# Optimization experiments

Hardware: AMD Instinct MI355X
Metric: run time of the kernel (lower is better)

Reference implementation:

```python
import jax, jax.numpy as jnp
import numpy as np
from jax.ops import segment_sum, segment_max

H, D, HID, L, B = 4, 32, 128, 2, 64  # heads, head_dim, hidden, layers, graphs
NB, NS, NC, NF = 100000, 20000, 10000, 2000


def setup_inputs() -> dict:
    key = jax.random.key(0)
    ks = iter(jax.random.split(key, 64))
    nrm = lambda shape, s=1.0: jax.random.normal(next(ks), shape, jnp.float32) * s
    ridx = lambda n, hi: jax.random.randint(next(ks), (n,), 0, hi, jnp.int32)
    srt = lambda n, hi: jnp.sort(jax.random.randint(next(ks), (n,), 0, hi, jnp.int32))
    return {
        'x_block': nrm((NB, 8)), 'x_spmt': nrm((NS, 10)),
        'x_crane': nrm((NC, 7)), 'x_facility': nrm((NF, 3)),
        'Wp_b': nrm((8, HID), 0.2), 'bp_b': jnp.zeros((HID,), jnp.float32),
        'Wp_s': nrm((10, HID), 0.2), 'bp_s': jnp.zeros((HID,), jnp.float32),
        'Wp_c': nrm((7, HID), 0.2), 'bp_c': jnp.zeros((HID,), jnp.float32),
        'Wp_f': nrm((3, HID), 0.2), 'bp_f': jnp.zeros((HID,), jnp.float32),
        'gat_W': nrm((L, 8, HID, HID), 0.05),
        'gat_as': nrm((L, 8, H, D), 0.1), 'gat_ad': nrm((L, 8, H, D), 0.1),
        'gat_b': jnp.zeros((L, 8, HID), jnp.float32),
        'ln_s': jnp.ones((L, HID), jnp.float32), 'ln_b': jnp.zeros((L, HID), jnp.float32),
        'e_nt_s': ridx(800000, NB), 'e_nt_d': ridx(800000, NS),
        'e_ct_s': ridx(800000, NS), 'e_ct_d': ridx(800000, NB),
        'e_nl_s': ridx(400000, NB), 'e_nl_d': ridx(400000, NC),
        'e_cl_s': ridx(400000, NC), 'e_cl_d': ridx(400000, NB),
        'e_ba_s': ridx(100000, NB), 'e_ba_d': ridx(100000, NF),
        'e_pr_s': ridx(800000, NB), 'e_pr_d': ridx(800000, NB),
        'e_sa_s': ridx(20000, NS), 'e_sa_d': ridx(20000, NF),
        'e_ca_s': ridx(10000, NC), 'e_ca_d': ridx(10000, NF),
        'b_block': srt(NB, B), 'b_spmt': srt(NS, B),
        'b_crane': srt(NC, B), 'b_facility': srt(NF, B),
    }


def layer_norm(x, s, b):
    mu = x.mean(-1, keepdims=True)
    v = ((x - mu) ** 2).mean(-1, keepdims=True)
    return (x - mu) / jnp.sqrt(v + 1e-5) * s + b


def gat(h_src, h_dst, src, dst, W, a_s, a_d, bias):
    # PyG GATConv (shared lin for src/dst, add_self_loops=False, eval mode)
    n_dst = h_dst.shape[0]
    hs = (h_src @ W).reshape(-1, H, D)                 # [Ns,H,D]
    hd = (h_dst @ W).reshape(-1, H, D)                 # [Nd,H,D]
    al_s = (hs * a_s).sum(-1)                          # [Ns,H]
    al_d = (hd * a_d).sum(-1)                          # [Nd,H]
    e = jax.nn.leaky_relu(al_s[src] + al_d[dst], 0.2)  # [E,H]
    m = segment_max(e, dst, num_segments=n_dst)
    m = jnp.where(jnp.isfinite(m), m, 0.0)             # empty segments
    ex = jnp.exp(e - m[dst])
    den = segment_sum(ex, dst, num_segments=n_dst)
    coef = ex / (den[dst] + 1e-16)                     # scatter-softmax
    msg = hs[src] * coef[..., None]                    # [E,H,D]
    out = segment_sum(msg, dst, num_segments=n_dst)
    return out.reshape(n_dst, H * D) + bias


def pool(x, b):
    s = segment_sum(x, b, num_segments=B)
    c = segment_sum(jnp.ones((x.shape[0],), x.dtype), b, num_segments=B)
    return s / jnp.clip(c, 1.0)[:, None]


def reference(x_block, x_spmt, x_crane, x_facility,
              Wp_b, bp_b, Wp_s, bp_s, Wp_c, bp_c, Wp_f, bp_f,
              gat_W, gat_as, gat_ad, gat_b, ln_s, ln_b,
              e_nt_s, e_nt_d, e_ct_s, e_ct_d, e_nl_s, e_nl_d, e_cl_s, e_cl_d,
              e_ba_s, e_ba_d, e_pr_s, e_pr_d, e_sa_s, e_sa_d, e_ca_s, e_ca_d,
              b_block, b_spmt, b_crane, b_facility):
    xb = x_block @ Wp_b + bp_b
    xs = x_spmt @ Wp_s + bp_s
    xc = x_crane @ Wp_c + bp_c
    xf = x_facility @ Wp_f + bp_f
    rels = [(0, 'b', 's', e_nt_s, e_nt_d), (1, 's', 'b', e_ct_s, e_ct_d),
            (2, 'b', 'c', e_nl_s, e_nl_d), (3, 'c', 'b', e_cl_s, e_cl_d),
            (4, 'b', 'f', e_ba_s, e_ba_d), (5, 'b', 'b', e_pr_s, e_pr_d),
            (6, 's', 'f', e_sa_s, e_sa_d), (7, 'c', 'f', e_ca_s, e_ca_d)]
    for l in range(L):
        x = {'b': xb, 's': xs, 'c': xc, 'f': xf}
        acc = {k: [] for k in x}
        for r, st, dt, src, dst in rels:
            acc[dt].append(gat(x[st], x[dt], src, dst,
                               gat_W[l, r], gat_as[l, r], gat_ad[l, r], gat_b[l, r]))
        new = {k: sum(v) / len(v) for k, v in acc.items()}  # HeteroConv mean
        xb = layer_norm(jax.nn.relu(new['b']) + xb, ln_s[l], ln_b[l])
        xs = layer_norm(jax.nn.relu(new['s']) + xs, ln_s[l], ln_b[l])
        xc = layer_norm(jax.nn.relu(new['c']) + xc, ln_s[l], ln_b[l])
        xf = layer_norm(jax.nn.relu(new['f']) + xf, ln_s[l], ln_b[l])
    return jnp.concatenate([pool(xb, b_block), pool(xs, b_spmt),
                            pool(xc, b_crane), pool(xf, b_facility)], axis=-1)
```

## Files before the change

### kernel.cpp

```cpp
#include <hip/hip_runtime.h>
#include <hip/hip_bf16.h>
#include <cstdint>

#define HID 128
#define NHEAD 4
#define NGRAPH 64
#define PCHUNK 32

typedef __attribute__((ext_vector_type(8))) short bf16x8;
typedef __attribute__((ext_vector_type(4))) short bf16x4s;
typedef __attribute__((ext_vector_type(4))) float f32x4;

__device__ __forceinline__ float bf2f(short u) {
    union { float f; unsigned int i; } c;
    c.i = ((unsigned int)(unsigned short)u) << 16;
    return c.f;
}
__device__ __forceinline__ float lrelu(float a) { return (a > 0.f) ? a : 0.2f * a; }

struct PrePack {
    const int* edst[8]; int* deg[8]; int E[8]; int h_off[9];
    const float* px[4]; const float* pW[4]; const float* pb[4]; float* po[4];
    int pN[4]; int pK[4]; int p_off[5];
    const float* gat_W; __hip_bfloat16* Wsw;
    const float* gat_as; const float* gat_ad; float* vecall;
};

__global__ __launch_bounds__(256) void k_pre(PrePack A) {
    int b = blockIdx.x;
    int tid = threadIdx.x;
    if (b < A.h_off[8]) {
#pragma unroll
        for (int r = 0; r < 8; ++r) {
            if (b >= A.h_off[r] && b < A.h_off[r + 1]) {
                int e = (b - A.h_off[r]) * 256 + tid;
                if (e < A.E[r]) atomicAdd(&A.deg[r][A.edst[r][e]], 1);
            }
        }
        return;
    }
    b -= A.h_off[8];
    if (b < A.p_off[4]) {
#pragma unroll
        for (int t = 0; t < 4; ++t) {
            if (b >= A.p_off[t] && b < A.p_off[t + 1]) {
                int idx = (b - A.p_off[t]) * 256 + tid;
                if (idx < A.pN[t] * HID) {
                    int row = idx >> 7, c = idx & 127;
                    int K = A.pK[t];
                    float acc = A.pb[t][c];
                    for (int k = 0; k < K; ++k) acc += A.px[t][row * K + k] * A.pW[t][k * HID + c];
                    A.po[t][idx] = acc;
                }
            }
        }
        return;
    }
    b -= A.p_off[4];
    if (b < 1024) {
        int idx = b * 256 + tid;
        int l = idx >> 17;
        int rem = idx & 131071;
        int k = rem >> 10;
        int gc = rem & 1023;
        int rel, n, gobase, Ncols;
        if (gc < 512) {
            int i = gc >> 7;
            rel = (i == 0) ? 0 : (i == 1) ? 2 : (i == 2) ? 4 : 5;
            n = gc; gobase = 0; Ncols = 512;
        } else if (gc < 768) {
            int c2 = gc - 512;
            rel = (c2 >> 7) ? 6 : 1;
            n = c2; gobase = 65536; Ncols = 256;
        } else {
            int c2 = gc - 768;
            rel = (c2 >> 7) ? 7 : 3;
            n = c2; gobase = 98304; Ncols = 256;
        }
        int nl = n & 127;
        float v = A.gat_W[(((size_t)l * 8 + rel) * 128 + k) * 128 + nl];
        size_t dst = (size_t)l * 131072 + gobase + ((size_t)(k >> 3) * Ncols + n) * 8 + (k & 7);
        A.Wsw[dst] = __float2bfloat16(v);
        return;
    }
    b -= 1024;
    {
        int idx = b * 256 + tid;
        if (idx < 16384) {
            int h = idx & 3, k = (idx >> 2) & 127, p = (idx >> 9) & 15, l = idx >> 13;
            int r = p >> 1, side = p & 1;
            const float* W = A.gat_W + (((size_t)l * 8 + r) * 128 + k) * 128;
            const float* a = (side ? A.gat_ad : A.gat_as) + ((size_t)l * 8 + r) * 128;
            float s = 0.f;
#pragma unroll
            for (int j = 0; j < 32; ++j) s += W[h * 32 + j] * a[h * 32 + j];
            A.vecall[((size_t)l * 16 + p) * 512 + k * 4 + h] = s;
        }
    }
}

struct CsrPack {
    const int* esrc[8];
    const int* edst[8];
    int* deg[8];
    int* offs[8];
    int* curs[8];
    int* adj[8];
    int E[8];
    int Nd[8];
};

__global__ void k_scan_part_all(CsrPack P, int* __restrict__ part_all) {
    int r = blockIdx.y;
    int N = P.Nd[r];
    if (blockIdx.x * 256 >= N) return;
    __shared__ int sh[256];
    int t = threadIdx.x, i = blockIdx.x * 256 + t;
    sh[t] = (i < N) ? P.deg[r][i] : 0;
    __syncthreads();
    for (int o = 128; o; o >>= 1) {
        if (t < o) sh[t] += sh[t + o];
        __syncthreads();
    }
    if (t == 0) part_all[r * 512 + blockIdx.x] = sh[0];
}
__global__ void k_scan_top_all(int* __restrict__ part_all, CsrPack P) {
    int r = blockIdx.x;
    int n = (P.Nd[r] + 255) / 256;
    __shared__ int sh[512];
    int t = threadIdx.x;
    int v = (t < n) ? part_all[r * 512 + t] : 0;
    sh[t] = v;
    __syncthreads();
    for (int o = 1; o < 512; o <<= 1) {
        int tmp = (t >= o) ? sh[t - o] : 0;
        __syncthreads();
        sh[t] += tmp;
        __syncthreads();
    }
    if (t < n) part_all[r * 512 + t] = sh[t] - v;
}
__global__ void k_scan_down_all(CsrPack P, const int* __restrict__ part_all) {
    int r = blockIdx.y;
    int N = P.Nd[r];
    if (blockIdx.x * 256 >= N) return;
    __shared__ int sh[256];
    int t = threadIdx.x, i = blockIdx.x * 256 + t;
    int v = (i < N) ? P.deg[r][i] : 0;
    sh[t] = v;
    __syncthreads();
    for (int o = 1; o < 256; o <<= 1) {
        int tmp = (t >= o) ? sh[t - o] : 0;
        __syncthreads();
        sh[t] += tmp;
        __syncthreads();
    }
    if (i < N) {
        int excl = sh[t] - v + part_all[r * 512 + blockIdx.x];
        P.offs[r][i] = excl;
        P.curs[r][i] = excl;
    }
}

struct BinPack {
    const int* esrc[8]; const int* edst[8];
    uint2* staging[8];
    int* curs[8]; int* adj[8];
    int* binCnt; int* binBase; int* binCur;
    int E[8]; int Nd[8]; int binshift[8];
};

__global__ void k_binscan(BinPack B, const int* __restrict__ part_all) {
    int r = threadIdx.x;
    if (r >= 8) return;
    int cnt[8];
#pragma unroll
    for (int b = 0; b < 8; ++b) cnt[b] = 0;
    int nparts = (B.Nd[r] + 255) >> 8;
    int cshift = B.binshift[r] - 8;
    for (int c = 0; c < nparts; ++c) cnt[c >> cshift] += part_all[r * 512 + c];
    int run = 0;
    for (int b = 0; b < 8; ++b) {
        B.binCnt[r * 8 + b] = cnt[b];
        B.binBase[r * 8 + b] = run;
        B.binCur[r * 8 + b] = run;
        run += cnt[b];
    }
}

__global__ __launch_bounds__(256) void k_binp1(BinPack B) {
    int r = blockIdx.y;
    int E = B.E[r];
    int sh = B.binshift[r];
    __shared__ int h[8], base[8], rk[8];
    int tid = threadIdx.x;
    for (int e0 = blockIdx.x * 256; e0 < E; e0 += gridDim.x * 256) {
        if (tid < 8) { h[tid] = 0; rk[tid] = 0; }
        __syncthreads();
        int e = e0 + tid;
        int valid = e < E;
        int src = 0, dst = 0, bin = 0;
        if (valid) {
            src = B.esrc[r][e];
            dst = B.edst[r][e];
            bin = dst >> sh;
            atomicAdd(&h[bin], 1);
        }
        __syncthreads();
        if (tid < 8 && h[tid] > 0) base[tid] = atomicAdd(&B.binCur[r * 8 + tid], h[tid]);
        __syncthreads();
        if (valid) {
            int pos = base[bin] + atomicAdd(&rk[bin], 1);
            B.staging[r][pos] = make_uint2((unsigned)src, (unsigned)dst);
        }
        __syncthreads();
    }
}

__global__ __launch_bounds__(256) void k_binp2(BinPack B) {
    int r = blockIdx.y;
    int bin = blockIdx.x & 7;
    int cstart = blockIdx.x >> 3;
    int nstride = gridDim.x >> 3;
    int cnt = B.binCnt[r * 8 + bin];
    const uint2* st = B.staging[r] + B.binBase[r * 8 + bin];
    int* curs = B.curs[r];
    int* adj = B.adj[r];
    for (int i0 = cstart * 256; i0 < cnt; i0 += nstride * 256) {
        int i = i0 + threadIdx.x;
        if (i < cnt) {
            uint2 ed = st[i];
            int slot = atomicAdd(&curs[ed.y], 1);
            adj[slot] = (int)ed.x;
        }
    }
}

__device__ __forceinline__ void gemm_body(char* smemraw, const float* __restrict__ A,
                                          const __hip_bfloat16* __restrict__ Bsw,
                                          __hip_bfloat16* __restrict__ out,
                                          int M, int Ncols, int bx, int by) {
    __hip_bfloat16 (*Alds)[136] = (__hip_bfloat16 (*)[136])smemraw;
    int m0 = bx * 64, n0 = by * 128;
    int t = threadIdx.x;
    for (int i = t; i < 2048; i += 256) {
        int row = i >> 5, ch = i & 31;
        float4 v = make_float4(0.f, 0.f, 0.f, 0.f);
        if (m0 + row < M) v = *(const float4*)(A + (size_t)(m0 + row) * 128 + ch * 4);
        __hip_bfloat16* dp = &Alds[row][ch * 4];
        dp[0] = __float2bfloat16(v.x);
        dp[1] = __float2bfloat16(v.y);
        dp[2] = __float2bfloat16(v.z);
        dp[3] = __float2bfloat16(v.w);
    }
    __syncthreads();
    int w = t >> 6, l = t & 63;
    int lane16 = l & 15, q = l >> 4;
    f32x4 acc[8];
#pragma unroll
    for (int nn = 0; nn < 8; ++nn) acc[nn] = (f32x4){0.f, 0.f, 0.f, 0.f};
    const __hip_bfloat16* arow = &Alds[w * 16 + lane16][q * 8];
#pragma unroll
    for (int kk = 0; kk < 4; ++kk) {
        bf16x8 a = *(const bf16x8*)(arow + kk * 32);
#pragma unroll
        for (int nn = 0; nn < 8; ++nn) {
            size_t boff = ((size_t)(kk * 4 + q) * Ncols + (n0 + nn * 16 + lane16)) * 8;
            bf16x8 b = *(const bf16x8*)(Bsw + boff);
            acc[nn] = __builtin_amdgcn_mfma_f32_16x16x32_bf16(a, b, acc[nn], 0, 0, 0);
        }
    }
    int orow = m0 + w * 16 + q * 4;
#pragma unroll
    for (int nn = 0; nn < 8; ++nn) {
        int col = n0 + nn * 16 + lane16;
#pragma unroll
        for (int r = 0; r < 4; ++r) {
            int row = orow + r;
            if (row < M) out[(size_t)row * Ncols + col] = __float2bfloat16(acc[nn][r]);
        }
    }
}

__device__ __forceinline__ void logits_body(char* smemraw,
                                            const float* const vec[7], float* const outp[7],
                                            const float* __restrict__ x, int N, int nv, int bloc) {
    float (*vs)[128][4] = (float (*)[128][4])smemraw;
    int t = threadIdx.x;
    for (int i = t; i < nv * 512; i += 256) {
        int v = i >> 9, j = i & 511;
        vs[v][j >> 2][j & 3] = vec[v][j];
    }
    __syncthreads();
    int nl = t >> 2, h = t & 3;
    int node = bloc * 64 + nl;
    if (node >= N) return;
    const float* xr = x + (size_t)node * 128;
    float acc[7];
#pragma unroll
    for (int v = 0; v < 7; ++v) acc[v] = 0.f;
#pragma unroll 4
    for (int k = 0; k < 128; ++k) {
        float xv = xr[k];
#pragma unroll
        for (int v = 0; v < 7; ++v)
            if (v < nv) acc[v] += xv * vs[v][k][h];
    }
#pragma unroll
    for (int v = 0; v < 7; ++v)
        if (v < nv) outp[v][node * 4 + h] = acc[v];
}

struct MidPack {
    const float* gA[3]; const __hip_bfloat16* gB[3]; __hip_bfloat16* gO[3];
    int gM[3]; int gNc[3]; int gMB[3]; int g_off[4];
    const float* lvec[4][7]; float* lout[4][7]; const float* lx[4];
    int lN[4]; int lnv[4]; int l_off[5];
};

__global__ __launch_bounds__(256) void k_mid(MidPack M) {
    __shared__ __align__(16) char smem[17408];
    int b = blockIdx.x;
    if (b < M.g_off[3]) {
#pragma unroll
        for (int g = 0; g < 3; ++g) {
            if (b >= M.g_off[g] && b < M.g_off[g + 1]) {
                int local = b - M.g_off[g];
                int bx = local % M.gMB[g];
                int by = local / M.gMB[g];
                gemm_body(smem, M.gA[g], M.gB[g], M.gO[g], M.gM[g], M.gNc[g], bx, by);
            }
        }
        return;
    }
    b -= M.g_off[3];
#pragma unroll
    for (int t = 0; t < 4; ++t) {
        if (b >= M.l_off[t] && b < M.l_off[t + 1]) {
            logits_body(smem, M.lvec[t], M.lout[t], M.lx[t], M.lN[t], M.lnv[t], b - M.l_off[t]);
        }
    }
}

struct RelArg {
    const __hip_bfloat16* hs;
    int hstride;
    int hoff;
    const float* als;
    const float* ald;
    const int* adj;
    const int* off;
    const int* deg;
    const float* bias;
};

__device__ __forceinline__ void dst_body(const RelArg& r0, const RelArg& r1, const RelArg& r2,
                                         int nrel, float inv_nrel, float* __restrict__ x,
                                         const float* __restrict__ ln_s,
                                         const float* __restrict__ ln_b, int N, int bloc) {
    int wv = threadIdx.x >> 6, lane = threadIdx.x & 63;
    int half = lane >> 5, sl = lane & 31;
    int d = bloc * 8 + wv * 2 + half;
    if (d >= N) return;
    int c0 = sl * 4;
    int h = sl >> 3;
    float4 xv = *(const float4*)&x[(size_t)d * HID + c0];
    float rel0 = 0.f, rel1 = 0.f, rel2 = 0.f, rel3 = 0.f;
    for (int rr = 0; rr < nrel; ++rr) {
        const RelArg& R = (rr == 0) ? r0 : (rr == 1) ? r1 : r2;
        int base = R.off[d];
        int dg = R.deg[d];
        float aldh = R.ald[d * NHEAD + h];
        const __hip_bfloat16* hp = R.hs + R.hoff + c0;
        const int hstr = R.hstride;
        const int* ap = R.adj + base;
        const float* als = R.als;
        float a0 = 0.f, a1 = 0.f, a2 = 0.f, a3 = 0.f, den = 0.f;
        int k = 0;
        for (; k + 4 <= dg; k += 4) {
            int s0 = ap[k], s1 = ap[k + 1], s2 = ap[k + 2], s3 = ap[k + 3];
            float w0 = __expf(lrelu(als[s0 * NHEAD + h] + aldh));
            float w1 = __expf(lrelu(als[s1 * NHEAD + h] + aldh));
            float w2 = __expf(lrelu(als[s2 * NHEAD + h] + aldh));
            float w3 = __expf(lrelu(als[s3 * NHEAD + h] + aldh));
            bf16x4s v0 = *(const bf16x4s*)(hp + (size_t)s0 * hstr);
            bf16x4s v1 = *(const bf16x4s*)(hp + (size_t)s1 * hstr);
            bf16x4s v2 = *(const bf16x4s*)(hp + (size_t)s2 * hstr);
            bf16x4s v3 = *(const bf16x4s*)(hp + (size_t)s3 * hstr);
            a0 += w0 * bf2f(v0[0]) + w1 * bf2f(v1[0]) + w2 * bf2f(v2[0]) + w3 * bf2f(v3[0]);
            a1 += w0 * bf2f(v0[1]) + w1 * bf2f(v1[1]) + w2 * bf2f(v2[1]) + w3 * bf2f(v3[1]);
            a2 += w0 * bf2f(v0[2]) + w1 * bf2f(v1[2]) + w2 * bf2f(v2[2]) + w3 * bf2f(v3[2]);
            a3 += w0 * bf2f(v0[3]) + w1 * bf2f(v1[3]) + w2 * bf2f(v2[3]) + w3 * bf2f(v3[3]);
            den += w0 + w1 + w2 + w3;
        }
        for (; k < dg; ++k) {
            int s = ap[k];
            float w = __expf(lrelu(als[s * NHEAD + h] + aldh));
            bf16x4s v = *(const bf16x4s*)(hp + (size_t)s * hstr);
            a0 += w * bf2f(v[0]);
            a1 += w * bf2f(v[1]);
            a2 += w * bf2f(v[2]);
            a3 += w * bf2f(v[3]);
            den += w;
        }
        float inv = 1.f / (den + 1e-16f);
        rel0 += a0 * inv + R.bias[c0];
        rel1 += a1 * inv + R.bias[c0 + 1];
        rel2 += a2 * inv + R.bias[c0 + 2];
        rel3 += a3 * inv + R.bias[c0 + 3];
    }
    float v0 = rel0 * inv_nrel, v1 = rel1 * inv_nrel;
    float v2 = rel2 * inv_nrel, v3 = rel3 * inv_nrel;
    v0 = (v0 > 0.f) ? v0 : 0.f;
    v1 = (v1 > 0.f) ? v1 : 0.f;
    v2 = (v2 > 0.f) ? v2 : 0.f;
    v3 = (v3 > 0.f) ? v3 : 0.f;
    v0 += xv.x; v1 += xv.y; v2 += xv.z; v3 += xv.w;
    float s = v0 + v1 + v2 + v3;
    float ss = v0 * v0 + v1 * v1 + v2 * v2 + v3 * v3;
#pragma unroll
    for (int o = 16; o; o >>= 1) {
        s += __shfl_xor(s, o);
        ss += __shfl_xor(ss, o);
    }
    float mu = s * (1.f / HID);
    float var = ss * (1.f / HID) - mu * mu;
    float rstd = rsqrtf(var + 1e-5f);
    float o0 = (v0 - mu) * rstd * ln_s[c0] + ln_b[c0];
    float o1 = (v1 - mu) * rstd * ln_s[c0 + 1] + ln_b[c0 + 1];
    float o2 = (v2 - mu) * rstd * ln_s[c0 + 2] + ln_b[c0 + 2];
    float o3 = (v3 - mu) * rstd * ln_s[c0 + 3] + ln_b[c0 + 3];
    *(float4*)&x[(size_t)d * HID + c0] = make_float4(o0, o1, o2, o3);
}

struct TypeArg {
    RelArg r0, r1, r2;
    float* x;
    int N;
    int nrel;
    float inv_nrel;
};

__global__ __launch_bounds__(256) void k_dst_all(TypeArg t0, TypeArg t1, TypeArg t2, TypeArg t3,
                                                 int off1, int off2, int off3,
                                                 const float* __restrict__ ln_s,
                                                 const float* __restrict__ ln_b) {
    int b = blockIdx.x;
    if (b < off1) {
        dst_body(t0.r0, t0.r1, t0.r2, t0.nrel, t0.inv_nrel, t0.x, ln_s, ln_b, t0.N, b);
    } else if (b < off2) {
        dst_body(t1.r0, t1.r1, t1.r2, t1.nrel, t1.inv_nrel, t1.x, ln_s, ln_b, t1.N, b - off1);
    } else if (b < off3) {
        dst_body(t2.r0, t2.r1, t2.r2, t2.nrel, t2.inv_nrel, t2.x, ln_s, ln_b, t2.N, b - off2);
    } else {
        dst_body(t3.r0, t3.r1, t3.r2, t3.nrel, t3.inv_nrel, t3.x, ln_s, ln_b, t3.N, b - off3);
    }
}

__global__ void k_pool_all(const float* __restrict__ x0, const float* __restrict__ x1,
                           const float* __restrict__ x2, const float* __restrict__ x3,
                           const int* __restrict__ b0, const int* __restrict__ b1,
                           const int* __restrict__ b2, const int* __restrict__ b3,
                           int N0, int N1, int N2, int N3, float* __restrict__ out) {
    int ty = blockIdx.y;
    const float* x;
    const int* b;
    int N, toff;
    if (ty == 0)      { x = x0; b = b0; N = N0; toff = 0; }
    else if (ty == 1) { x = x1; b = b1; N = N1; toff = 128; }
    else if (ty == 2) { x = x2; b = b2; N = N2; toff = 256; }
    else              { x = x3; b = b3; N = N3; toff = 384; }
    int r0 = blockIdx.x * PCHUNK;
    if (r0 >= N) return;
    int rend = min(r0 + PCHUNK, N);
    int c = threadIdx.x;
    int cur = b[r0];
    float acc = 0.f;
    for (int i = r0; i < rend; ++i) {
        int g = b[i];
        if (g != cur) {
            atomicAdd(&out[cur * 512 + toff + c], acc);
            acc = 0.f;
            cur = g;
        }
        acc += x[(size_t)i * HID + c];
    }
    atomicAdd(&out[cur * 512 + toff + c], acc);
}
__global__ void k_cnt(const int* __restrict__ b0, const int* __restrict__ b1,
                      const int* __restrict__ b2, const int* __restrict__ b3,
                      int N0, int N1, int N2, int N3, float* __restrict__ cnt) {
    int i = blockIdx.x * blockDim.x + threadIdx.x;
    if (i >= 256) return;
    int t = i >> 6, g = i & 63;
    const int* b = (t == 0) ? b0 : (t == 1) ? b1 : (t == 2) ? b2 : b3;
    int N = (t == 0) ? N0 : (t == 1) ? N1 : (t == 2) ? N2 : N3;
    int lo = 0, hi = N;
    while (lo < hi) { int m = (lo + hi) >> 1; if (b[m] < g) lo = m + 1; else hi = m; }
    int s = lo;
    hi = N;
    while (lo < hi) { int m = (lo + hi) >> 1; if (b[m] < g + 1) lo = m + 1; else hi = m; }
    cnt[i] = (float)(lo - s);
}
__global__ void k_div(float* __restrict__ out, const float* __restrict__ cnt) {
    int idx = blockIdx.x * blockDim.x + threadIdx.x;
    if (idx >= NGRAPH * 512) return;
    int g = idx >> 9, c = idx & 511, t = c >> 7;
    out[idx] = out[idx] / fmaxf(cnt[t * NGRAPH + g], 1.0f);
}

extern "C" void kernel_launch(void* const* d_in, const int* in_sizes, int n_in,
                              void* d_out, int out_size, void* d_ws, size_t ws_size,
                              hipStream_t stream) {
    const float* x_in[4] = {(const float*)d_in[0], (const float*)d_in[1],
                            (const float*)d_in[2], (const float*)d_in[3]};
    const float* Wp[4] = {(const float*)d_in[4], (const float*)d_in[6],
                          (const float*)d_in[8], (const float*)d_in[10]};
    const float* bp[4] = {(const float*)d_in[5], (const float*)d_in[7],
                          (const float*)d_in[9], (const float*)d_in[11]};
    const float* gat_W  = (const float*)d_in[12];
    const float* gat_as = (const float*)d_in[13];
    const float* gat_ad = (const float*)d_in[14];
    const float* gat_b  = (const float*)d_in[15];
    const float* ln_s   = (const float*)d_in[16];
    const float* ln_b   = (const float*)d_in[17];
    const int* esrc[8] = {(const int*)d_in[18], (const int*)d_in[20], (const int*)d_in[22],
                          (const int*)d_in[24], (const int*)d_in[26], (const int*)d_in[28],
                          (const int*)d_in[30], (const int*)d_in[32]};
    const int* edst[8] = {(const int*)d_in[19], (const int*)d_in[21], (const int*)d_in[23],
                          (const int*)d_in[25], (const int*)d_in[27], (const int*)d_in[29],
                          (const int*)d_in[31], (const int*)d_in[33]};
    const int* bidx[4] = {(const int*)d_in[34], (const int*)d_in[35],
                          (const int*)d_in[36], (const int*)d_in[37]};
    int E[8];
    {
        const int eidx[8] = {18, 20, 22, 24, 26, 28, 30, 32};
        for (int r = 0; r < 8; ++r) E[r] = in_sizes[eidx[r]];
    }
    const int Kin[4] = {8, 10, 7, 3};
    int N[4];
    for (int t = 0; t < 4; ++t) N[t] = in_sizes[t] / Kin[t];
    const int rel_st[8] = {0, 1, 0, 2, 0, 0, 1, 2};
    const int rel_dt[8] = {1, 0, 2, 0, 3, 0, 3, 3};
    const int rel_hoff[8] = {0, 0, 128, 0, 256, 384, 128, 128};
    const int grp_stride[4] = {512, 256, 256, 0};
    (void)ws_size; (void)n_in;

    char* wbase = (char*)d_ws;
    size_t cur = 0;
    auto alloc = [&](size_t bytes) -> void* {
        void* p = wbase + cur;
        cur += (bytes + 15) & ~(size_t)15;
        return p;
    };
    float* x[4];
    for (int t = 0; t < 4; ++t) x[t] = (float*)alloc((size_t)N[t] * HID * 4);
    __hip_bfloat16* hs_g[3];
    hs_g[0] = (__hip_bfloat16*)alloc((size_t)N[0] * 512 * 2);
    hs_g[1] = (__hip_bfloat16*)alloc((size_t)N[1] * 256 * 2);
    hs_g[2] = (__hip_bfloat16*)alloc((size_t)N[2] * 256 * 2);
    __hip_bfloat16* Wsw = (__hip_bfloat16*)alloc((size_t)2 * 131072 * 2);
    float* vecall = (float*)alloc((size_t)2 * 16 * 512 * 4);
    float *als_[8], *ald_[8];
    int *deg[8], *offs[8], *curs[8], *adj[8];
    uint2* staging[8];
    int NdTot = 0;
    for (int r = 0; r < 8; ++r) NdTot += N[rel_dt[r]] + 4;
    int* deg_all = (int*)alloc((size_t)NdTot * 4);
    {
        int off = 0;
        for (int r = 0; r < 8; ++r) { deg[r] = deg_all + off; off += N[rel_dt[r]] + 4; }
    }
    for (int r = 0; r < 8; ++r) {
        int Ns = N[rel_st[r]], Nd = N[rel_dt[r]];
        als_[r] = (float*)alloc((size_t)Ns * NHEAD * 4);
        ald_[r] = (float*)alloc((size_t)Nd * NHEAD * 4);
        offs[r] = (int*)alloc((size_t)Nd * 4);
        curs[r] = (int*)alloc((size_t)Nd * 4);
        adj[r]  = (int*)alloc((size_t)E[r] * 4);
        staging[r] = (uint2*)alloc((size_t)E[r] * 8);
    }
    int* part_all = (int*)alloc(8 * 512 * 4);
    int* binCnt   = (int*)alloc(64 * 4);
    int* binBase  = (int*)alloc(64 * 4);
    int* binCur   = (int*)alloc(64 * 4);
    float* cntf   = (float*)alloc(256 * 4);

    CsrPack CP;
    int NdMax = 0, Emax = 0;
    for (int r = 0; r < 8; ++r) {
        CP.esrc[r] = esrc[r]; CP.edst[r] = edst[r];
        CP.deg[r] = deg[r]; CP.offs[r] = offs[r]; CP.curs[r] = curs[r]; CP.adj[r] = adj[r];
        CP.E[r] = E[r]; CP.Nd[r] = N[rel_dt[r]];
        if (CP.Nd[r] > NdMax) NdMax = CP.Nd[r];
        if (E[r] > Emax) Emax = E[r];
    }
    BinPack BP;
    for (int r = 0; r < 8; ++r) {
        BP.esrc[r] = esrc[r]; BP.edst[r] = edst[r];
        BP.staging[r] = staging[r];
        BP.curs[r] = curs[r]; BP.adj[r] = adj[r];
        BP.E[r] = E[r]; BP.Nd[r] = N[rel_dt[r]];
        int sh = 8;
        while (((BP.Nd[r] - 1) >> sh) > 7) ++sh;
        BP.binshift[r] = sh;
    }
    BP.binCnt = binCnt; BP.binBase = binBase; BP.binCur = binCur;

    hipMemsetAsync(deg_all, 0, (size_t)NdTot * 4, stream);
    PrePack PA;
    {
        for (int r = 0; r < 8; ++r) { PA.edst[r] = edst[r]; PA.deg[r] = deg[r]; PA.E[r] = E[r]; }
        PA.h_off[0] = 0;
        for (int r = 0; r < 8; ++r) PA.h_off[r + 1] = PA.h_off[r] + (E[r] + 255) / 256;
        for (int t = 0; t < 4; ++t) {
            PA.px[t] = x_in[t]; PA.pW[t] = Wp[t]; PA.pb[t] = bp[t]; PA.po[t] = x[t];
            PA.pN[t] = N[t]; PA.pK[t] = Kin[t];
        }
        PA.p_off[0] = 0;
        for (int t = 0; t < 4; ++t) PA.p_off[t + 1] = PA.p_off[t] + (N[t] * HID + 255) / 256;
        PA.gat_W = gat_W; PA.Wsw = Wsw;
        PA.gat_as = gat_as; PA.gat_ad = gat_ad; PA.vecall = vecall;
        int total = PA.h_off[8] + PA.p_off[4] + 1024 + 64;
        k_pre<<<total, 256, 0, stream>>>(PA);
    }

    {
        dim3 gn((NdMax + 255) / 256, 8);
        k_scan_part_all<<<gn, 256, 0, stream>>>(CP, part_all);
        k_binscan<<<1, 64, 0, stream>>>(BP, part_all);
        k_scan_top_all<<<8, 512, 0, stream>>>(part_all, CP);
        k_scan_down_all<<<gn, 256, 0, stream>>>(CP, part_all);
        dim3 g1(512, 8);
        k_binp1<<<g1, 256, 0, stream>>>(BP);
        dim3 g2(512, 8);
        k_binp2<<<g2, 256, 0, stream>>>(BP);
    }

    hipMemsetAsync(d_out, 0, (size_t)out_size * 4, stream);
    k_cnt<<<1, 256, 0, stream>>>(bidx[0], bidx[1], bidx[2], bidx[3],
                                 N[0], N[1], N[2], N[3], cntf);

    const size_t g_woff[3] = {0, 65536, 98304};
    const int g_ncols[3] = {512, 256, 256};
    int nb[4];
    for (int t = 0; t < 4; ++t) nb[t] = (N[t] + 7) / 8;
    int doff1 = nb[0], doff2 = nb[0] + nb[1], doff3 = nb[0] + nb[1] + nb[2];
    int dtot = doff3 + nb[3];

    for (int l = 0; l < 2; ++l) {
        MidPack M;
        M.g_off[0] = 0;
        for (int g = 0; g < 3; ++g) {
            M.gA[g] = x[g];
            M.gB[g] = Wsw + (size_t)l * 131072 + g_woff[g];
            M.gO[g] = hs_g[g];
            M.gM[g] = N[g];
            M.gNc[g] = g_ncols[g];
            M.gMB[g] = (N[g] + 63) / 64;
            M.g_off[g + 1] = M.g_off[g] + M.gMB[g] * (g_ncols[g] / 128);
        }
        const float* vl = vecall + (size_t)l * 16 * 512;
        auto vvec = [&](int r, int side) { return vl + (size_t)(r * 2 + side) * 512; };
        for (int t = 0; t < 4; ++t)
            for (int v = 0; v < 7; ++v) { M.lvec[t][v] = vl; M.lout[t][v] = als_[0]; }
        M.lvec[0][0] = vvec(0, 0); M.lout[0][0] = als_[0];
        M.lvec[0][1] = vvec(2, 0); M.lout[0][1] = als_[2];
        M.lvec[0][2] = vvec(4, 0); M.lout[0][2] = als_[4];
        M.lvec[0][3] = vvec(5, 0); M.lout[0][3] = als_[5];
        M.lvec[0][4] = vvec(1, 1); M.lout[0][4] = ald_[1];
        M.lvec[0][5] = vvec(3, 1); M.lout[0][5] = ald_[3];
        M.lvec[0][6] = vvec(5, 1); M.lout[0][6] = ald_[5];
        M.lvec[1][0] = vvec(1, 0); M.lout[1][0] = als_[1];
        M.lvec[1][1] = vvec(6, 0); M.lout[1][1] = als_[6];
        M.lvec[1][2] = vvec(0, 1); M.lout[1][2] = ald_[0];
        M.lvec[2][0] = vvec(3, 0); M.lout[2][0] = als_[3];
        M.lvec[2][1] = vvec(7, 0); M.lout[2][1] = als_[7];
        M.lvec[2][2] = vvec(2, 1); M.lout[2][2] = ald_[2];
        M.lvec[3][0] = vvec(4, 1); M.lout[3][0] = ald_[4];
        M.lvec[3][1] = vvec(6, 1); M.lout[3][1] = ald_[6];
        M.lvec[3][2] = vvec(7, 1); M.lout[3][2] = ald_[7];
        const int lnv[4] = {7, 3, 3, 3};
        M.l_off[0] = 0;
        for (int t = 0; t < 4; ++t) {
            M.lx[t] = x[t]; M.lN[t] = N[t]; M.lnv[t] = lnv[t];
            M.l_off[t + 1] = M.l_off[t] + (N[t] + 63) / 64;
        }
        int total = M.g_off[3] + M.l_off[4];
        k_mid<<<total, 256, 0, stream>>>(M);

        auto mk = [&](int r) {
            RelArg a;
            int st = rel_st[r];
            a.hs = hs_g[st]; a.hstride = grp_stride[st]; a.hoff = rel_hoff[r];
            a.als = als_[r]; a.ald = ald_[r];
            a.adj = adj[r]; a.off = offs[r]; a.deg = deg[r];
            a.bias = gat_b + (size_t)(l * 8 + r) * HID;
            return a;
        };
        TypeArg T[4];
        const int trels[4][3] = {{1, 3, 5}, {0, 0, 0}, {2, 2, 2}, {4, 6, 7}};
        const int tnrel[4] = {3, 1, 1, 3};
        const float tinv[4] = {1.f / 3.f, 1.f, 1.f, 1.f / 3.f};
        for (int t = 0; t < 4; ++t) {
            T[t].r0 = mk(trels[t][0]);
            T[t].r1 = mk(trels[t][1]);
            T[t].r2 = mk(trels[t][2]);
            T[t].x = x[t];
            T[t].N = N[t];
            T[t].nrel = tnrel[t];
            T[t].inv_nrel = tinv[t];
        }
        k_dst_all<<<dtot, 256, 0, stream>>>(T[0], T[1], T[2], T[3], doff1, doff2, doff3,
                                            ln_s + l * HID, ln_b + l * HID);
    }

    {
        int pmax = 0;
        for (int t = 0; t < 4; ++t) {
            int p = (N[t] + PCHUNK - 1) / PCHUNK;
            if (p > pmax) pmax = p;
        }
        dim3 gp(pmax, 4);
        k_pool_all<<<gp, 128, 0, stream>>>(x[0], x[1], x[2], x[3],
                                           bidx[0], bidx[1], bidx[2], bidx[3],
                                           N[0], N[1], N[2], N[3], (float*)d_out);
    }
    k_div<<<(NGRAPH * 512 + 255) / 256, 256, 0, stream>>>((float*)d_out, cntf);
}
```

Measured before the change: 1.384 ms.

## Build CSR via per-bin LDS histograms and LDS cursors instead of global atomics

Degree counting moves from global per-destination atomics to a coarse 8-bin histogram in k_pre, followed by per-bin LDS histograms after edges are staged into bins. The CSR fill (k_binp2) now keeps its cursors in shared memory, one 1024-thread block per bin. This is meant to cut global atomic contention and traffic during the graph preprocessing. The trade-off is only 64 blocks for the histogram and fill stages, which limits parallelism, plus a reordered kernel chain and a 64 KB LDS array per block.

```diff
diff --git a/kernel.cpp b/kernel.cpp
--- a/kernel.cpp
+++ b/kernel.cpp
@@ -6,6 +6,7 @@
 #define NHEAD 4
 #define NGRAPH 64
 #define PCHUNK 32
+#define MAXBINW 16384
 
 typedef __attribute__((ext_vector_type(8))) short bf16x8;
 typedef __attribute__((ext_vector_type(4))) short bf16x4s;
@@ -19,7 +20,8 @@
 __device__ __forceinline__ float lrelu(float a) { return (a > 0.f) ? a : 0.2f * a; }
 
 struct PrePack {
-    const int* edst[8]; int* deg[8]; int E[8]; int h_off[9];
+    const int* edst[8]; int E[8]; int h_off[9]; int bsh[8];
+    int* binCnt;
     const float* px[4]; const float* pW[4]; const float* pb[4]; float* po[4];
     int pN[4]; int pK[4]; int p_off[5];
     const float* gat_W; __hip_bfloat16* Wsw;
@@ -30,11 +32,16 @@
     int b = blockIdx.x;
     int tid = threadIdx.x;
     if (b < A.h_off[8]) {
+        __shared__ int h8[8];
+        if (tid < 8) h8[tid] = 0;
+        __syncthreads();
 #pragma unroll
         for (int r = 0; r < 8; ++r) {
             if (b >= A.h_off[r] && b < A.h_off[r + 1]) {
                 int e = (b - A.h_off[r]) * 256 + tid;
-                if (e < A.E[r]) atomicAdd(&A.deg[r][A.edst[r][e]], 1);
+                if (e < A.E[r]) atomicAdd(&h8[A.edst[r][e] >> A.bsh[r]], 1);
+                __syncthreads();
+                if (tid < 8 && h8[tid] > 0) atomicAdd(&A.binCnt[r * 8 + tid], h8[tid]);
             }
         }
         return;
@@ -99,18 +106,106 @@
     }
 }
 
-struct CsrPack {
-    const int* esrc[8];
-    const int* edst[8];
+struct BinPack {
+    const int* esrc[8]; const int* edst[8];
+    uint2* staging[8];
+    int* adj[8]; int* deg[8]; int* offs[8];
+    int* binCnt; int* binBase; int* binCur;
+    int E[8]; int Nd[8]; int binshift[8];
+};
+
+__global__ void k_binscan2(BinPack B) {
+    int r = threadIdx.x;
+    if (r >= 8) return;
+    int run = 0;
+    for (int b = 0; b < 8; ++b) {
+        int c = B.binCnt[r * 8 + b];
+        B.binBase[r * 8 + b] = run;
+        B.binCur[r * 8 + b] = run;
+        run += c;
+    }
+}
+
+__global__ __launch_bounds__(256) void k_binp1(BinPack B) {
+    int r = blockIdx.y;
+    int E = B.E[r];
+    int sh = B.binshift[r];
+    __shared__ int h[8], base[8], rk[8];
+    int tid = threadIdx.x;
+    for (int e0 = blockIdx.x * 256; e0 < E; e0 += gridDim.x * 256) {
+        if (tid < 8) { h[tid] = 0; rk[tid] = 0; }
+        __syncthreads();
+        int e = e0 + tid;
+        int valid = e < E;
+        int src = 0, dst = 0, bin = 0;
+        if (valid) {
+            src = B.esrc[r][e];
+            dst = B.edst[r][e];
+            bin = dst >> sh;
+            atomicAdd(&h[bin], 1);
+        }
+        __syncthreads();
+        if (tid < 8 && h[tid] > 0) base[tid] = atomicAdd(&B.binCur[r * 8 + tid], h[tid]);
+        __syncthreads();
+        if (valid) {
+            int pos = base[bin] + atomicAdd(&rk[bin], 1);
+            B.staging[r][pos] = make_uint2((unsigned)src, (unsigned)dst);
+        }
+        __syncthreads();
+    }
+}
+
+__global__ __launch_bounds__(1024) void k_binhist(BinPack B) {
+    int r = blockIdx.y, bin = blockIdx.x;
+    int sh = B.binshift[r];
+    int width = 1 << sh;
+    int d0 = bin << sh;
+    int Nd = B.Nd[r];
+    int ndst = Nd - d0;
+    if (ndst > width) ndst = width;
+    __shared__ int h[MAXBINW];
+    int tid = threadIdx.x;
+    for (int i = tid; i < width; i += 1024) h[i] = 0;
+    __syncthreads();
+    if (ndst > 0) {
+        int cnt = B.binCnt[r * 8 + bin];
+        const uint2* st = B.staging[r] + B.binBase[r * 8 + bin];
+        for (int i = tid; i < cnt; i += 1024) atomicAdd(&h[(int)st[i].y - d0], 1);
+        __syncthreads();
+        for (int i = tid; i < ndst; i += 1024) B.deg[r][d0 + i] = h[i];
+    }
+}
+
+__global__ __launch_bounds__(1024) void k_binp2(BinPack B) {
+    int r = blockIdx.y, bin = blockIdx.x;
+    int sh = B.binshift[r];
+    int width = 1 << sh;
+    int d0 = bin << sh;
+    int Nd = B.Nd[r];
+    int ndst = Nd - d0;
+    if (ndst > width) ndst = width;
+    if (ndst <= 0) return;
+    __shared__ int curs[MAXBINW];
+    int tid = threadIdx.x;
+    for (int i = tid; i < ndst; i += 1024) curs[i] = B.offs[r][d0 + i];
+    __syncthreads();
+    int cnt = B.binCnt[r * 8 + bin];
+    const uint2* st = B.staging[r] + B.binBase[r * 8 + bin];
+    int* adj = B.adj[r];
+    for (int i = tid; i < cnt; i += 1024) {
+        uint2 ed = st[i];
+        int slot = atomicAdd(&curs[(int)ed.y - d0], 1);
+        adj[slot] = (int)ed.x;
+    }
+}
+
+struct ScanPack {
     int* deg[8];
     int* offs[8];
-    int* curs[8];
-    int* adj[8];
-    int E[8];
     int Nd[8];
 };
 
-__global__ void k_scan_part_all(CsrPack P, int* __restrict__ part_all) {
+__global__ void k_scan_part_all(ScanPack P, int* __restrict__ part_all) {
     int r = blockIdx.y;
     int N = P.Nd[r];
     if (blockIdx.x * 256 >= N) return;
@@ -124,7 +219,7 @@
     }
     if (t == 0) part_all[r * 512 + blockIdx.x] = sh[0];
 }
-__global__ void k_scan_top_all(int* __restrict__ part_all, CsrPack P) {
+__global__ void k_scan_top_all(int* __restrict__ part_all, ScanPack P) {
     int r = blockIdx.x;
     int n = (P.Nd[r] + 255) / 256;
     __shared__ int sh[512];
@@ -140,7 +235,7 @@
     }
     if (t < n) part_all[r * 512 + t] = sh[t] - v;
 }
-__global__ void k_scan_down_all(CsrPack P, const int* __restrict__ part_all) {
+__global__ void k_scan_down_all(ScanPack P, const int* __restrict__ part_all) {
     int r = blockIdx.y;
     int N = P.Nd[r];
     if (blockIdx.x * 256 >= N) return;
@@ -155,85 +250,7 @@
         sh[t] += tmp;
         __syncthreads();
     }
-    if (i < N) {
-        int excl = sh[t] - v + part_all[r * 512 + blockIdx.x];
-        P.offs[r][i] = excl;
-        P.curs[r][i] = excl;
-    }
-}
-
-struct BinPack {
-    const int* esrc[8]; const int* edst[8];
-    uint2* staging[8];
-    int* curs[8]; int* adj[8];
-    int* binCnt; int* binBase; int* binCur;
-    int E[8]; int Nd[8]; int binshift[8];
-};
-
-__global__ void k_binscan(BinPack B, const int* __restrict__ part_all) {
-    int r = threadIdx.x;
-    if (r >= 8) return;
-    int cnt[8];
-#pragma unroll
-    for (int b = 0; b < 8; ++b) cnt[b] = 0;
-    int nparts = (B.Nd[r] + 255) >> 8;
-    int cshift = B.binshift[r] - 8;
-    for (int c = 0; c < nparts; ++c) cnt[c >> cshift] += part_all[r * 512 + c];
-    int run = 0;
-    for (int b = 0; b < 8; ++b) {
-        B.binCnt[r * 8 + b] = cnt[b];
-        B.binBase[r * 8 + b] = run;
-        B.binCur[r * 8 + b] = run;
-        run += cnt[b];
-    }
-}
-
-__global__ __launch_bounds__(256) void k_binp1(BinPack B) {
-    int r = blockIdx.y;
-    int E = B.E[r];
-    int sh = B.binshift[r];
-    __shared__ int h[8], base[8], rk[8];
-    int tid = threadIdx.x;
-    for (int e0 = blockIdx.x * 256; e0 < E; e0 += gridDim.x * 256) {
-        if (tid < 8) { h[tid] = 0; rk[tid] = 0; }
-        __syncthreads();
-        int e = e0 + tid;
-        int valid = e < E;
-        int src = 0, dst = 0, bin = 0;
-        if (valid) {
-            src = B.esrc[r][e];
-            dst = B.edst[r][e];
-            bin = dst >> sh;
-            atomicAdd(&h[bin], 1);
-        }
-        __syncthreads();
-        if (tid < 8 && h[tid] > 0) base[tid] = atomicAdd(&B.binCur[r * 8 + tid], h[tid]);
-        __syncthreads();
-        if (valid) {
-            int pos = base[bin] + atomicAdd(&rk[bin], 1);
-            B.staging[r][pos] = make_uint2((unsigned)src, (unsigned)dst);
-        }
-        __syncthreads();
-    }
-}
-
-__global__ __launch_bounds__(256) void k_binp2(BinPack B) {
-    int r = blockIdx.y;
-    int bin = blockIdx.x & 7;
-    int cstart = blockIdx.x >> 3;
-    int nstride = gridDim.x >> 3;
-    int cnt = B.binCnt[r * 8 + bin];
-    const uint2* st = B.staging[r] + B.binBase[r * 8 + bin];
-    int* curs = B.curs[r];
-    int* adj = B.adj[r];
-    for (int i0 = cstart * 256; i0 < cnt; i0 += nstride * 256) {
-        int i = i0 + threadIdx.x;
-        if (i < cnt) {
-            uint2 ed = st[i];
-            int slot = atomicAdd(&curs[ed.y], 1);
-            adj[slot] = (int)ed.x;
-        }
-    }
+    if (i < N) P.offs[r][i] = sh[t] - v + part_all[r * 512 + blockIdx.x];
 }
 
 __device__ __forceinline__ void gemm_body(char* smemraw, const float* __restrict__ A,
@@ -562,21 +579,14 @@
     __hip_bfloat16* Wsw = (__hip_bfloat16*)alloc((size_t)2 * 131072 * 2);
     float* vecall = (float*)alloc((size_t)2 * 16 * 512 * 4);
     float *als_[8], *ald_[8];
-    int *deg[8], *offs[8], *curs[8], *adj[8];
+    int *deg[8], *offs[8], *adj[8];
     uint2* staging[8];
-    int NdTot = 0;
-    for (int r = 0; r < 8; ++r) NdTot += N[rel_dt[r]] + 4;
-    int* deg_all = (int*)alloc((size_t)NdTot * 4);
-    {
-        int off = 0;
-        for (int r = 0; r < 8; ++r) { deg[r] = deg_all + off; off += N[rel_dt[r]] + 4; }
-    }
     for (int r = 0; r < 8; ++r) {
         int Ns = N[rel_st[r]], Nd = N[rel_dt[r]];
         als_[r] = (float*)alloc((size_t)Ns * NHEAD * 4);
         ald_[r] = (float*)alloc((size_t)Nd * NHEAD * 4);
+        deg[r]  = (int*)alloc((size_t)Nd * 4);
         offs[r] = (int*)alloc((size_t)Nd * 4);
-        curs[r] = (int*)alloc((size_t)Nd * 4);
         adj[r]  = (int*)alloc((size_t)E[r] * 4);
         staging[r] = (uint2*)alloc((size_t)E[r] * 8);
     }
@@ -586,31 +596,27 @@
     int* binCur   = (int*)alloc(64 * 4);
     float* cntf   = (float*)alloc(256 * 4);
 
-    CsrPack CP;
-    int NdMax = 0, Emax = 0;
-    for (int r = 0; r < 8; ++r) {
-        CP.esrc[r] = esrc[r]; CP.edst[r] = edst[r];
-        CP.deg[r] = deg[r]; CP.offs[r] = offs[r]; CP.curs[r] = curs[r]; CP.adj[r] = adj[r];
-        CP.E[r] = E[r]; CP.Nd[r] = N[rel_dt[r]];
-        if (CP.Nd[r] > NdMax) NdMax = CP.Nd[r];
-        if (E[r] > Emax) Emax = E[r];
-    }
     BinPack BP;
+    int NdMax = 0;
     for (int r = 0; r < 8; ++r) {
         BP.esrc[r] = esrc[r]; BP.edst[r] = edst[r];
         BP.staging[r] = staging[r];
-        BP.curs[r] = curs[r]; BP.adj[r] = adj[r];
+        BP.adj[r] = adj[r]; BP.deg[r] = deg[r]; BP.offs[r] = offs[r];
         BP.E[r] = E[r]; BP.Nd[r] = N[rel_dt[r]];
         int sh = 8;
         while (((BP.Nd[r] - 1) >> sh) > 7) ++sh;
         BP.binshift[r] = sh;
+        if (BP.Nd[r] > NdMax) NdMax = BP.Nd[r];
     }
     BP.binCnt = binCnt; BP.binBase = binBase; BP.binCur = binCur;
-
-    hipMemsetAsync(deg_all, 0, (size_t)NdTot * 4, stream);
+    ScanPack SP;
+    for (int r = 0; r < 8; ++r) { SP.deg[r] = deg[r]; SP.offs[r] = offs[r]; SP.Nd[r] = BP.Nd[r]; }
+
+    hipMemsetAsync(binCnt, 0, 64 * 4, stream);
     PrePack PA;
     {
-        for (int r = 0; r < 8; ++r) { PA.edst[r] = edst[r]; PA.deg[r] = deg[r]; PA.E[r] = E[r]; }
+        for (int r = 0; r < 8; ++r) { PA.edst[r] = edst[r]; PA.E[r] = E[r]; PA.bsh[r] = BP.binshift[r]; }
+        PA.binCnt = binCnt;
         PA.h_off[0] = 0;
         for (int r = 0; r < 8; ++r) PA.h_off[r + 1] = PA.h_off[r] + (E[r] + 255) / 256;
         for (int t = 0; t < 4; ++t) {
@@ -626,15 +632,16 @@
     }
 
     {
-        dim3 gn((NdMax + 255) / 256, 8);
-        k_scan_part_all<<<gn, 256, 0, stream>>>(CP, part_all);
-        k_binscan<<<1, 64, 0, stream>>>(BP, part_all);
-        k_scan_top_all<<<8, 512, 0, stream>>>(part_all, CP);
-        k_scan_down_all<<<gn, 256, 0, stream>>>(CP, part_all);
+        k_binscan2<<<1, 64, 0, stream>>>(BP);
         dim3 g1(512, 8);
         k_binp1<<<g1, 256, 0, stream>>>(BP);
-        dim3 g2(512, 8);
-        k_binp2<<<g2, 256, 0, stream>>>(BP);
+        dim3 gb(8, 8);
+        k_binhist<<<gb, 1024, 0, stream>>>(BP);
+        dim3 gn((NdMax + 255) / 256, 8);
+        k_scan_part_all<<<gn, 256, 0, stream>>>(SP, part_all);
+        k_scan_top_all<<<8, 512, 0, stream>>>(part_all, SP);
+        k_scan_down_all<<<gn, 256, 0, stream>>>(SP, part_all);
+        k_binp2<<<gb, 1024, 0, stream>>>(BP);
     }
 
     hipMemsetAsync(d_out, 0, (size_t)out_size * 4, stream);
```

Measured after the change: 1.386 ms. About the same (+0.2%).
